# Kernel tuning notes

Measured on AMD Instinct MI355X. Metric: run time of the kernel, lower is better.

Reference implementation:

```python
import jax, jax.numpy as jnp
import numpy as np

N = 50000       # n_nodes
E = 800000      # n_edges
DIN = 64
DH = 64
DOUT = 64


def setup_inputs() -> dict:
    key = jax.random.key(0)
    k0, k1, k2, k3, k4 = jax.random.split(key, 5)
    x = jax.random.normal(k0, (N, DIN), dtype=jnp.float32)
    edge_index = jax.random.randint(k1, (2, E), 0, N, dtype=jnp.int32)
    # learnable per-edge weight (nn.Parameter); positive init keeps gcn_norm well-defined
    edge_weight = jax.random.uniform(k2, (E,), jnp.float32, 0.1, 1.0)
    W1 = jax.random.normal(k3, (DH, DIN), dtype=jnp.float32) * (1.0 / np.sqrt(DIN))
    b1 = jnp.zeros((DH,), jnp.float32)
    W2 = jax.random.normal(k4, (DOUT, DH), dtype=jnp.float32) * (1.0 / np.sqrt(DH))
    b2 = jnp.zeros((DOUT,), jnp.float32)
    return {"x": x, "edge_weight": edge_weight, "W1": W1, "b1": b1,
            "W2": W2, "b2": b2, "edge_index": edge_index}


def _gcn_norm(edge_index, edge_weight, n):
    # PyG gcn_norm: add self-loops (weight 1), symmetric normalization.
    loop = jnp.arange(n, dtype=edge_index.dtype)
    row = jnp.concatenate([edge_index[0], loop])   # source nodes
    col = jnp.concatenate([edge_index[1], loop])   # target nodes
    w = jnp.concatenate([edge_weight, jnp.ones((n,), edge_weight.dtype)])
    deg = jax.ops.segment_sum(w, col, num_segments=n)
    dinv = jnp.where(deg > 0, jax.lax.rsqrt(jnp.where(deg > 0, deg, 1.0)), 0.0)
    norm = dinv[row] * w * dinv[col]               # [E + N]
    return row, col, norm


def _gcn_layer(x, W, b, row, col, norm, n):
    h = x @ W.T                                     # [N, out]
    # gather source features, scale by norm, scatter-add into targets
    out = jax.ops.segment_sum(h[row] * norm[:, None], col, num_segments=n)
    return out + b


def reference(x, edge_weight, W1, b1, W2, b2, edge_index):
    n = x.shape[0]
    row, col, norm = _gcn_norm(edge_index, edge_weight, n)
    h = _gcn_layer(x, W1, b1, row, col, norm, n)
    h = jax.nn.relu(h)                              # self.pre: ReLU + Dropout (identity in eval)
    return _gcn_layer(h, W2, b2, row, col, norm, n)
```

## Files before the change

### kernel.cpp

```cpp
#include <hip/hip_runtime.h>

#define D 64
#define GN 128
#define SW 68
#define SX 132
#define MAXDEG 64

typedef unsigned long long u64;
typedef unsigned int u32;
typedef unsigned short u16;

__device__ __forceinline__ float4 fma4(float4 w, float s, float4 c) {
    c.x = fmaf(w.x, s, c.x); c.y = fmaf(w.y, s, c.y);
    c.z = fmaf(w.z, s, c.z); c.w = fmaf(w.w, s, c.w);
    return c;
}

__device__ __forceinline__ u32 f2bf(float f) {
    u32 u = __float_as_uint(f);
    return (u + 0x7FFFu + ((u >> 16) & 1u)) >> 16;
}
__device__ __forceinline__ u32 pack2(float a, float b) { return f2bf(a) | (f2bf(b) << 16); }
__device__ __forceinline__ float blo(u32 u) { return __uint_as_float(u << 16); }
__device__ __forceinline__ float bhi(u32 u) { return __uint_as_float(u & 0xFFFF0000u); }

__device__ __forceinline__ float decdeg(u64 dc) {
    return (float)(u32)dc * (1.0f / 16777216.0f) + 1.0f;
}

template<bool RELU_IN, bool DO_EDGES>
__global__ __launch_bounds__(256) void k_gemm(
        const float* __restrict__ in, const float* __restrict__ W,
        u16* __restrict__ h, int N,
        const int* __restrict__ ei, const float* __restrict__ ew,
        u64* __restrict__ degcnt, int2* __restrict__ eg, int E, int epb) {
    __shared__ __align__(16) float sWt[D * SW];
    __shared__ __align__(16) float sxT[D * SX];

    int t = threadIdx.x;
    int node0 = blockIdx.x * GN;

    if (DO_EDGES) {
        int ebeg = blockIdx.x * epb;
        int eend = min(ebeg + epb, E);
        for (int e = ebeg + t; e < eend; e += 256) {
            int r   = ei[e];
            int c   = ei[(size_t)E + e];
            float w = ew[e];
            u64 packed = (1ULL << 32) | (u64)(u32)(w * 16777216.0f);
            u64 old = atomicAdd(&degcnt[c], packed);
            u32 rank = (u32)(old >> 32);
            if (rank < MAXDEG)
                eg[((size_t)c << 6) + rank] = make_int2(r, __float_as_int(w));
        }
    }

    for (int i = t; i < D * D / 4; i += 256) {
        int j = i >> 4, k4 = i & 15;
        float4 w = ((const float4*)W)[i];
        sWt[(4 * k4 + 0) * SW + j] = w.x;
        sWt[(4 * k4 + 1) * SW + j] = w.y;
        sWt[(4 * k4 + 2) * SW + j] = w.z;
        sWt[(4 * k4 + 3) * SW + j] = w.w;
    }
    for (int i = t; i < GN * D / 4; i += 256) {
        int nn = i >> 4, k4 = i & 15;
        int n = node0 + nn;
        float4 v = make_float4(0.f, 0.f, 0.f, 0.f);
        if (n < N) v = ((const float4*)(in + (size_t)n * D))[k4];
        if (RELU_IN) {
            v.x = fmaxf(v.x, 0.f); v.y = fmaxf(v.y, 0.f);
            v.z = fmaxf(v.z, 0.f); v.w = fmaxf(v.w, 0.f);
        }
        sxT[(4 * k4 + 0) * SX + nn] = v.x;
        sxT[(4 * k4 + 1) * SX + nn] = v.y;
        sxT[(4 * k4 + 2) * SX + nn] = v.z;
        sxT[(4 * k4 + 3) * SX + nn] = v.w;
    }
    __syncthreads();

    int jg = (t & 7) * 8;
    int ng = (t >> 3) * 4;
    float4 a0[4], a1[4];
    #pragma unroll
    for (int a = 0; a < 4; ++a) {
        a0[a] = make_float4(0.f, 0.f, 0.f, 0.f);
        a1[a] = make_float4(0.f, 0.f, 0.f, 0.f);
    }

    #pragma unroll 8
    for (int k = 0; k < D; ++k) {
        const float* wr = &sWt[k * SW + jg];
        float4 w0 = *(const float4*)wr;
        float4 w1 = *(const float4*)(wr + 4);
        float4 xv = *(const float4*)&sxT[k * SX + ng];
        a0[0] = fma4(w0, xv.x, a0[0]);  a1[0] = fma4(w1, xv.x, a1[0]);
        a0[1] = fma4(w0, xv.y, a0[1]);  a1[1] = fma4(w1, xv.y, a1[1]);
        a0[2] = fma4(w0, xv.z, a0[2]);  a1[2] = fma4(w1, xv.z, a1[2]);
        a0[3] = fma4(w0, xv.w, a0[3]);  a1[3] = fma4(w1, xv.w, a1[3]);
    }

    #pragma unroll
    for (int a = 0; a < 4; ++a) {
        int n = node0 + ng + a;
        if (n >= N) continue;
        uint4 st;
        st.x = pack2(a0[a].x, a0[a].y);
        st.y = pack2(a0[a].z, a0[a].w);
        st.z = pack2(a1[a].x, a1[a].y);
        st.w = pack2(a1[a].z, a1[a].w);
        *(uint4*)(h + (size_t)n * D + jg) = st;
    }
}

__global__ __launch_bounds__(256) void k_aggregate(
        const u16* __restrict__ h, const u64* __restrict__ degcnt,
        const int2* __restrict__ eg, const float* __restrict__ b,
        float* __restrict__ out, int N) {
    int t = threadIdx.x;
    int n = blockIdx.x * 4 + (t >> 6);
    if (n >= N) return;
    int lane = t & 63;
    int g = lane >> 3;
    int f = (lane & 7) * 8;

    u64 dcn = degcnt[n];
    int c = min((int)(dcn >> 32), MAXDEG);
    float dinv_n = rsqrtf(decdeg(dcn));

    float acc[8] = {0.f, 0.f, 0.f, 0.f, 0.f, 0.f, 0.f, 0.f};
    if (g == 0) {
        float d2 = dinv_n * dinv_n;
        uint4 hv = *(const uint4*)(h + ((size_t)n << 6) + f);
        float4 b0 = *(const float4*)(b + f);
        float4 b1 = *(const float4*)(b + f + 4);
        acc[0] = fmaf(blo(hv.x), d2, b0.x); acc[1] = fmaf(bhi(hv.x), d2, b0.y);
        acc[2] = fmaf(blo(hv.y), d2, b0.z); acc[3] = fmaf(bhi(hv.y), d2, b0.w);
        acc[4] = fmaf(blo(hv.z), d2, b1.x); acc[5] = fmaf(bhi(hv.z), d2, b1.y);
        acc[6] = fmaf(blo(hv.w), d2, b1.z); acc[7] = fmaf(bhi(hv.w), d2, b1.w);
    }

    size_t s = (size_t)n << 6;
    int i = g;
    for (; i + 8 < c; i += 16) {
        int2 e0 = eg[s + i];
        int2 e1 = eg[s + i + 8];
        u64 d0 = degcnt[e0.x];
        u64 d1 = degcnt[e1.x];
        uint4 h0 = *(const uint4*)(h + ((size_t)e0.x << 6) + f);
        uint4 h1 = *(const uint4*)(h + ((size_t)e1.x << 6) + f);
        float w0 = __int_as_float(e0.y) * dinv_n * rsqrtf(decdeg(d0));
        float w1 = __int_as_float(e1.y) * dinv_n * rsqrtf(decdeg(d1));
        acc[0] = fmaf(blo(h0.x), w0, acc[0]); acc[1] = fmaf(bhi(h0.x), w0, acc[1]);
        acc[2] = fmaf(blo(h0.y), w0, acc[2]); acc[3] = fmaf(bhi(h0.y), w0, acc[3]);
        acc[4] = fmaf(blo(h0.z), w0, acc[4]); acc[5] = fmaf(bhi(h0.z), w0, acc[5]);
        acc[6] = fmaf(blo(h0.w), w0, acc[6]); acc[7] = fmaf(bhi(h0.w), w0, acc[7]);
        acc[0] = fmaf(blo(h1.x), w1, acc[0]); acc[1] = fmaf(bhi(h1.x), w1, acc[1]);
        acc[2] = fmaf(blo(h1.y), w1, acc[2]); acc[3] = fmaf(bhi(h1.y), w1, acc[3]);
        acc[4] = fmaf(blo(h1.z), w1, acc[4]); acc[5] = fmaf(bhi(h1.z), w1, acc[5]);
        acc[6] = fmaf(blo(h1.w), w1, acc[6]); acc[7] = fmaf(bhi(h1.w), w1, acc[7]);
    }
    if (i < c) {
        int2 e0 = eg[s + i];
        u64 d0 = degcnt[e0.x];
        uint4 h0 = *(const uint4*)(h + ((size_t)e0.x << 6) + f);
        float w0 = __int_as_float(e0.y) * dinv_n * rsqrtf(decdeg(d0));
        acc[0] = fmaf(blo(h0.x), w0, acc[0]); acc[1] = fmaf(bhi(h0.x), w0, acc[1]);
        acc[2] = fmaf(blo(h0.y), w0, acc[2]); acc[3] = fmaf(bhi(h0.y), w0, acc[3]);
        acc[4] = fmaf(blo(h0.z), w0, acc[4]); acc[5] = fmaf(bhi(h0.z), w0, acc[5]);
        acc[6] = fmaf(blo(h0.w), w0, acc[6]); acc[7] = fmaf(bhi(h0.w), w0, acc[7]);
    }

    #pragma unroll
    for (int k = 0; k < 8; ++k) {
        acc[k] += __shfl_xor(acc[k], 8);
        acc[k] += __shfl_xor(acc[k], 16);
        acc[k] += __shfl_xor(acc[k], 32);
    }

    if (g == 0) {
        float4* o = (float4*)(out + ((size_t)n << 6) + f);
        o[0] = make_float4(acc[0], acc[1], acc[2], acc[3]);
        o[1] = make_float4(acc[4], acc[5], acc[6], acc[7]);
    }
}

extern "C" void kernel_launch(void* const* d_in, const int* in_sizes, int n_in,
                              void* d_out, int out_size, void* d_ws, size_t ws_size,
                              hipStream_t stream) {
    const float* x  = (const float*)d_in[0];
    const float* ew = (const float*)d_in[1];
    const float* W1 = (const float*)d_in[2];
    const float* b1 = (const float*)d_in[3];
    const float* W2 = (const float*)d_in[4];
    const float* b2 = (const float*)d_in[5];
    const int*   ei = (const int*)d_in[6];

    int N = in_sizes[0] / D;
    int E = in_sizes[1];
    float* out = (float*)d_out;

    char* p = (char*)d_ws;
    u64*   degcnt = (u64*)p;   p += (size_t)N * 8;
    int2*  eg     = (int2*)p;  p += (size_t)N * MAXDEG * 8;
    u16*   h      = (u16*)p;   p += (size_t)N * D * 2;
    float* agg1   = (float*)p; p += (size_t)N * D * 4;

    dim3 blk(256);
    int gemm_grid = (N + GN - 1) / GN;
    int epb = (E + gemm_grid - 1) / gemm_grid;
    int agg_grid = (N + 3) / 4;

    hipMemsetAsync(degcnt, 0, (size_t)N * 8, stream);

    k_gemm<false, true><<<dim3(gemm_grid), blk, 0, stream>>>(
        x, W1, h, N, ei, ew, degcnt, eg, E, epb);
    k_aggregate<<<dim3(agg_grid), blk, 0, stream>>>(h, degcnt, eg, b1, agg1, N);

    k_gemm<true, false><<<dim3(gemm_grid), blk, 0, stream>>>(
        agg1, W2, h, N, nullptr, nullptr, nullptr, nullptr, 0, 0);
    k_aggregate<<<dim3(agg_grid), blk, 0, stream>>>(h, degcnt, eg, b2, out, N);
}
```

Baseline: 207.7 us.

## Split edge bucketing into sharded counters in a separate kernel, remap GEMM loads

Edge bucketing moves out of the first GEMM into its own one-thread-per-edge kernel. Each target node now has two atomic counters, picked by edge parity, each with a 32-slot sub-bucket, so contention on a single counter is halved. The aggregate kernel reads both counters, sums their degrees, and walks both sub-buckets interleaved. The GEMM staging loops are also re-indexed so consecutive threads write consecutive shared-memory addresses. The cost is an extra kernel launch, an extra degcnt load per gathered edge, and the loss of the overlap between edge processing and the GEMM; an unbalanced parity split can also drop edges earlier than the old 64-slot limit.

```diff
diff --git a/kernel.cpp b/kernel.cpp
--- a/kernel.cpp
+++ b/kernel.cpp
@@ -4,7 +4,7 @@
 #define GN 128
 #define SW 68
 #define SX 132
-#define MAXDEG 64
+#define SHSLOT 32
 
 typedef unsigned long long u64;
 typedef unsigned int u32;
@@ -24,58 +24,53 @@
 __device__ __forceinline__ float blo(u32 u) { return __uint_as_float(u << 16); }
 __device__ __forceinline__ float bhi(u32 u) { return __uint_as_float(u & 0xFFFF0000u); }
 
-__device__ __forceinline__ float decdeg(u64 dc) {
-    return (float)(u32)dc * (1.0f / 16777216.0f) + 1.0f;
-}
-
-template<bool RELU_IN, bool DO_EDGES>
+__global__ __launch_bounds__(256) void k_edges(
+        const int* __restrict__ ei, const float* __restrict__ ew,
+        u64* __restrict__ degcnt, int2* __restrict__ eg, int E) {
+    int e = blockIdx.x * blockDim.x + threadIdx.x;
+    if (e >= E) return;
+    int r = ei[e];
+    int c = ei[(size_t)E + e];
+    float w = ew[e];
+    int sh = e & 1;
+    u64 packed = (1ULL << 32) | (u64)(u32)(w * 16777216.0f);
+    u64 old = atomicAdd(&degcnt[2 * c + sh], packed);
+    u32 rank = (u32)(old >> 32);
+    if (rank < SHSLOT)
+        eg[((size_t)c << 6) + (sh << 5) + rank] = make_int2(r, __float_as_int(w));
+}
+
+template<bool RELU_IN>
 __global__ __launch_bounds__(256) void k_gemm(
         const float* __restrict__ in, const float* __restrict__ W,
-        u16* __restrict__ h, int N,
-        const int* __restrict__ ei, const float* __restrict__ ew,
-        u64* __restrict__ degcnt, int2* __restrict__ eg, int E, int epb) {
+        u16* __restrict__ h, int N) {
     __shared__ __align__(16) float sWt[D * SW];
     __shared__ __align__(16) float sxT[D * SX];
 
     int t = threadIdx.x;
     int node0 = blockIdx.x * GN;
 
-    if (DO_EDGES) {
-        int ebeg = blockIdx.x * epb;
-        int eend = min(ebeg + epb, E);
-        for (int e = ebeg + t; e < eend; e += 256) {
-            int r   = ei[e];
-            int c   = ei[(size_t)E + e];
-            float w = ew[e];
-            u64 packed = (1ULL << 32) | (u64)(u32)(w * 16777216.0f);
-            u64 old = atomicAdd(&degcnt[c], packed);
-            u32 rank = (u32)(old >> 32);
-            if (rank < MAXDEG)
-                eg[((size_t)c << 6) + rank] = make_int2(r, __float_as_int(w));
-        }
-    }
-
     for (int i = t; i < D * D / 4; i += 256) {
-        int j = i >> 4, k4 = i & 15;
-        float4 w = ((const float4*)W)[i];
-        sWt[(4 * k4 + 0) * SW + j] = w.x;
-        sWt[(4 * k4 + 1) * SW + j] = w.y;
-        sWt[(4 * k4 + 2) * SW + j] = w.z;
-        sWt[(4 * k4 + 3) * SW + j] = w.w;
+        int j = i & 63, kq = i >> 6;
+        float4 w = ((const float4*)W)[j * 16 + kq];
+        sWt[(4 * kq + 0) * SW + j] = w.x;
+        sWt[(4 * kq + 1) * SW + j] = w.y;
+        sWt[(4 * kq + 2) * SW + j] = w.z;
+        sWt[(4 * kq + 3) * SW + j] = w.w;
     }
     for (int i = t; i < GN * D / 4; i += 256) {
-        int nn = i >> 4, k4 = i & 15;
+        int nn = i & 127, kq = i >> 7;
         int n = node0 + nn;
         float4 v = make_float4(0.f, 0.f, 0.f, 0.f);
-        if (n < N) v = ((const float4*)(in + (size_t)n * D))[k4];
+        if (n < N) v = ((const float4*)(in + (size_t)n * D))[kq];
         if (RELU_IN) {
             v.x = fmaxf(v.x, 0.f); v.y = fmaxf(v.y, 0.f);
             v.z = fmaxf(v.z, 0.f); v.w = fmaxf(v.w, 0.f);
         }
-        sxT[(4 * k4 + 0) * SX + nn] = v.x;
-        sxT[(4 * k4 + 1) * SX + nn] = v.y;
-        sxT[(4 * k4 + 2) * SX + nn] = v.z;
-        sxT[(4 * k4 + 3) * SX + nn] = v.w;
+        sxT[(4 * kq + 0) * SX + nn] = v.x;
+        sxT[(4 * kq + 1) * SX + nn] = v.y;
+        sxT[(4 * kq + 2) * SX + nn] = v.z;
+        sxT[(4 * kq + 3) * SX + nn] = v.w;
     }
     __syncthreads();
 
@@ -113,6 +108,22 @@
     }
 }
 
+__device__ __forceinline__ void do_edge(float acc[8], const u16* __restrict__ h,
+                                        const u64* __restrict__ degcnt,
+                                        const int2* __restrict__ eg,
+                                        size_t slot, float dinv_n, int f) {
+    int2 e = eg[slot];
+    u64 da = degcnt[2 * e.x];
+    u64 db = degcnt[2 * e.x + 1];
+    uint4 hv = *(const uint4*)(h + ((size_t)e.x << 6) + f);
+    float degr = (float)((u32)da + (u32)db) * (1.0f / 16777216.0f) + 1.0f;
+    float w = __int_as_float(e.y) * dinv_n * rsqrtf(degr);
+    acc[0] = fmaf(blo(hv.x), w, acc[0]); acc[1] = fmaf(bhi(hv.x), w, acc[1]);
+    acc[2] = fmaf(blo(hv.y), w, acc[2]); acc[3] = fmaf(bhi(hv.y), w, acc[3]);
+    acc[4] = fmaf(blo(hv.z), w, acc[4]); acc[5] = fmaf(bhi(hv.z), w, acc[5]);
+    acc[6] = fmaf(blo(hv.w), w, acc[6]); acc[7] = fmaf(bhi(hv.w), w, acc[7]);
+}
+
 __global__ __launch_bounds__(256) void k_aggregate(
         const u16* __restrict__ h, const u64* __restrict__ degcnt,
         const int2* __restrict__ eg, const float* __restrict__ b,
@@ -124,9 +135,11 @@
     int g = lane >> 3;
     int f = (lane & 7) * 8;
 
-    u64 dcn = degcnt[n];
-    int c = min((int)(dcn >> 32), MAXDEG);
-    float dinv_n = rsqrtf(decdeg(dcn));
+    u64 d0 = degcnt[2 * n];
+    u64 d1 = degcnt[2 * n + 1];
+    int c0 = min((int)(d0 >> 32), SHSLOT);
+    int c1 = min((int)(d1 >> 32), SHSLOT);
+    float dinv_n = rsqrtf((float)((u32)d0 + (u32)d1) * (1.0f / 16777216.0f) + 1.0f);
 
     float acc[8] = {0.f, 0.f, 0.f, 0.f, 0.f, 0.f, 0.f, 0.f};
     if (g == 0) {
@@ -140,36 +153,14 @@
         acc[6] = fmaf(blo(hv.w), d2, b1.z); acc[7] = fmaf(bhi(hv.w), d2, b1.w);
     }
 
-    size_t s = (size_t)n << 6;
-    int i = g;
-    for (; i + 8 < c; i += 16) {
-        int2 e0 = eg[s + i];
-        int2 e1 = eg[s + i + 8];
-        u64 d0 = degcnt[e0.x];
-        u64 d1 = degcnt[e1.x];
-        uint4 h0 = *(const uint4*)(h + ((size_t)e0.x << 6) + f);
-        uint4 h1 = *(const uint4*)(h + ((size_t)e1.x << 6) + f);
-        float w0 = __int_as_float(e0.y) * dinv_n * rsqrtf(decdeg(d0));
-        float w1 = __int_as_float(e1.y) * dinv_n * rsqrtf(decdeg(d1));
-        acc[0] = fmaf(blo(h0.x), w0, acc[0]); acc[1] = fmaf(bhi(h0.x), w0, acc[1]);
-        acc[2] = fmaf(blo(h0.y), w0, acc[2]); acc[3] = fmaf(bhi(h0.y), w0, acc[3]);
-        acc[4] = fmaf(blo(h0.z), w0, acc[4]); acc[5] = fmaf(bhi(h0.z), w0, acc[5]);
-        acc[6] = fmaf(blo(h0.w), w0, acc[6]); acc[7] = fmaf(bhi(h0.w), w0, acc[7]);
-        acc[0] = fmaf(blo(h1.x), w1, acc[0]); acc[1] = fmaf(bhi(h1.x), w1, acc[1]);
-        acc[2] = fmaf(blo(h1.y), w1, acc[2]); acc[3] = fmaf(bhi(h1.y), w1, acc[3]);
-        acc[4] = fmaf(blo(h1.z), w1, acc[4]); acc[5] = fmaf(bhi(h1.z), w1, acc[5]);
-        acc[6] = fmaf(blo(h1.w), w1, acc[6]); acc[7] = fmaf(bhi(h1.w), w1, acc[7]);
-    }
-    if (i < c) {
-        int2 e0 = eg[s + i];
-        u64 d0 = degcnt[e0.x];
-        uint4 h0 = *(const uint4*)(h + ((size_t)e0.x << 6) + f);
-        float w0 = __int_as_float(e0.y) * dinv_n * rsqrtf(decdeg(d0));
-        acc[0] = fmaf(blo(h0.x), w0, acc[0]); acc[1] = fmaf(bhi(h0.x), w0, acc[1]);
-        acc[2] = fmaf(blo(h0.y), w0, acc[2]); acc[3] = fmaf(bhi(h0.y), w0, acc[3]);
-        acc[4] = fmaf(blo(h0.z), w0, acc[4]); acc[5] = fmaf(bhi(h0.z), w0, acc[5]);
-        acc[6] = fmaf(blo(h0.w), w0, acc[6]); acc[7] = fmaf(bhi(h0.w), w0, acc[7]);
-    }
+    size_t base = (size_t)n << 6;
+    int i0 = g, i1 = g;
+    for (; i0 < c0 && i1 < c1; i0 += 8, i1 += 8) {
+        do_edge(acc, h, degcnt, eg, base + i0, dinv_n, f);
+        do_edge(acc, h, degcnt, eg, base + 32 + i1, dinv_n, f);
+    }
+    for (; i0 < c0; i0 += 8) do_edge(acc, h, degcnt, eg, base + i0, dinv_n, f);
+    for (; i1 < c1; i1 += 8) do_edge(acc, h, degcnt, eg, base + 32 + i1, dinv_n, f);
 
     #pragma unroll
     for (int k = 0; k < 8; ++k) {
@@ -201,23 +192,21 @@
     float* out = (float*)d_out;
 
     char* p = (char*)d_ws;
-    u64*   degcnt = (u64*)p;   p += (size_t)N * 8;
-    int2*  eg     = (int2*)p;  p += (size_t)N * MAXDEG * 8;
+    u64*   degcnt = (u64*)p;   p += (size_t)N * 16;
+    int2*  eg     = (int2*)p;  p += (size_t)N * 64 * 8;
     u16*   h      = (u16*)p;   p += (size_t)N * D * 2;
     float* agg1   = (float*)p; p += (size_t)N * D * 4;
 
     dim3 blk(256);
     int gemm_grid = (N + GN - 1) / GN;
-    int epb = (E + gemm_grid - 1) / gemm_grid;
-    int agg_grid = (N + 3) / 4;
-
-    hipMemsetAsync(degcnt, 0, (size_t)N * 8, stream);
-
-    k_gemm<false, true><<<dim3(gemm_grid), blk, 0, stream>>>(
-        x, W1, h, N, ei, ew, degcnt, eg, E, epb);
+    int agg_grid  = (N + 3) / 4;
+
+    hipMemsetAsync(degcnt, 0, (size_t)N * 16, stream);
+    k_edges<<<dim3((E + 255) / 256), blk, 0, stream>>>(ei, ew, degcnt, eg, E);
+
+    k_gemm<false><<<dim3(gemm_grid), blk, 0, stream>>>(x, W1, h, N);
     k_aggregate<<<dim3(agg_grid), blk, 0, stream>>>(h, degcnt, eg, b1, agg1, N);
 
-    k_gemm<true, false><<<dim3(gemm_grid), blk, 0, stream>>>(
-        agg1, W2, h, N, nullptr, nullptr, nullptr, nullptr, 0, 0);
+    k_gemm<true><<<dim3(gemm_grid), blk, 0, stream>>>(agg1, W2, h, N);
     k_aggregate<<<dim3(agg_grid), blk, 0, stream>>>(h, degcnt, eg, b2, out, N);
 }
```

After: 212.4 us. 1.02x slower.
